# Optimization experiments

Measured on AMD Instinct MI355X. Metric: run time of the kernel, lower is better.

Reference implementation:

```python
import jax, jax.numpy as jnp
import numpy as np

B, N, H, TD = 64, 100, 128, 128
EPS = 1e-5  # BatchNorm eps (torch default)


def _xavier(k, shape):
    fan_in, fan_out = shape
    lim = (6.0 / (fan_in + fan_out)) ** 0.5
    return jax.random.uniform(k, shape, jnp.float32, -lim, lim)


def setup_inputs() -> dict:
    key = jax.random.key(0)
    ks = jax.random.split(key, 12)
    inp = {}
    inp["X"] = jax.random.randint(ks[0], (B, N * N), 0, 2).astype(jnp.float32)
    inp["time"] = jax.random.uniform(ks[1], (B,), jnp.float32)
    # Time_embedding MLP: Linear(TD->H), ReLU, Linear(H->H)
    inp["Wt1"] = _xavier(ks[2], (TD, H)); inp["bt1"] = jnp.zeros((H,), jnp.float32)
    inp["Wt2"] = _xavier(ks[3], (H, H)); inp["bt2"] = jnp.zeros((H,), jnp.float32)
    # TemporalGCNBlock.time_emb: Linear(H->N) + BN(N) + ReLU
    inp["Wtn"] = _xavier(ks[4], (H, N)); inp["btn"] = jnp.zeros((N,), jnp.float32)
    inp["g_tn"] = jnp.ones((N,), jnp.float32); inp["b_tn"] = jnp.zeros((N,), jnp.float32)
    # three GCNConv layers + BN
    inp["Wg1"] = _xavier(ks[5], (2 * N, H)); inp["bg1"] = jnp.zeros((H,), jnp.float32)
    inp["g1"] = jnp.ones((H,), jnp.float32); inp["bb1"] = jnp.zeros((H,), jnp.float32)
    inp["Wg2"] = _xavier(ks[6], (H, H)); inp["bg2"] = jnp.zeros((H,), jnp.float32)
    inp["g2"] = jnp.ones((H,), jnp.float32); inp["bb2"] = jnp.zeros((H,), jnp.float32)
    inp["Wg3"] = _xavier(ks[7], (H, H)); inp["bg3"] = jnp.zeros((H,), jnp.float32)
    inp["g3"] = jnp.ones((H,), jnp.float32); inp["bb3"] = jnp.zeros((H,), jnp.float32)
    # edge head: Linear(2H->H)+BN(H), Linear(2H->1)+BN(1)
    inp["We0"] = _xavier(ks[8], (2 * H, H)); inp["be0"] = jnp.zeros((H,), jnp.float32)
    inp["g_e0"] = jnp.ones((H,), jnp.float32); inp["b_e0"] = jnp.zeros((H,), jnp.float32)
    inp["We1"] = _xavier(ks[9], (2 * H, 1)); inp["be1"] = jnp.zeros((1,), jnp.float32)
    inp["g_e1"] = jnp.ones((1,), jnp.float32); inp["b_e1"] = jnp.zeros((1,), jnp.float32)
    return inp


def _bn(x, g, b):
    # eval-mode BatchNorm with fresh running stats (mean=0, var=1)
    return g * (x / jnp.sqrt(1.0 + EPS)) + b


def _timestep_embedding(t, dim, max_positions=10000):
    half = dim // 2
    freqs = jnp.exp(jnp.arange(half, dtype=jnp.float32) * (-np.log(max_positions) / (half - 1)))
    ang = t[:, None] * freqs[None, :]  # (B, half)
    return jnp.concatenate([jnp.sin(ang), jnp.cos(ang)], axis=1)


def reference(X, time, Wt1, bt1, Wt2, bt2, Wtn, btn, g_tn, b_tn,
              Wg1, bg1, g1, bb1, Wg2, bg2, g2, bb2, Wg3, bg3, g3, bb3,
              We0, be0, g_e0, b_e0, We1, be1, g_e1, b_e1):
    eye = jnp.eye(N, dtype=jnp.float32)
    # dense_to_sparse keeps nonzeros with unit edge weight; gcn_norm adds
    # remaining self-loops then symmetric-normalizes: A_hat = D^-1/2 (A|I) D^-1/2
    A = (X.reshape(B, N, N) != 0).astype(jnp.float32)
    At = jnp.maximum(A, eye)
    dinv = At.sum(-1) ** -0.5  # deg >= 1 thanks to self-loops
    Ah = dinv[:, :, None] * At * dinv[:, None, :]  # (B,N,N)

    # global time embedding (B,H)
    temb = _timestep_embedding(time, TD)
    h = jax.nn.relu(temb @ Wt1 + bt1) @ Wt2 + bt2
    # per-node time features (B,N); repeat_interleave == same vector per node
    t_node = jax.nn.relu(_bn(h @ Wtn + btn, g_tn, b_tn))
    x = jnp.concatenate([jnp.broadcast_to(eye, (B, N, N)),
                         jnp.broadcast_to(t_node[:, None, :], (B, N, N))], axis=-1)  # (B,N,2N)

    def gcn_block(x, W, b, g, bb):
        return jax.nn.relu(_bn(jnp.einsum('bij,bjh->bih', Ah, x @ W) + b, g, bb))

    x = gcn_block(x, Wg1, bg1, g1, bb1)
    x = gcn_block(x, Wg2, bg2, g2, bb2)
    x = gcn_block(x, Wg3, bg3, g3, bb3)  # (B,N,H)

    # edge head: Linear on concat(x_i, x_j) == split projections + broadcast add
    ei = x @ We0[:H]          # (B,N,H)
    ej = x @ We0[H:]          # (B,N,H)
    e0 = ei[:, :, None, :] + ej[:, None, :, :] + be0  # (B,N,N,H)
    e0 = _bn(e0, g_e0, b_e0)
    # Linear on concat(e0, time_emb): split into edge and time projections
    s = jnp.einsum('bijh,h->bij', e0, We1[:H, 0]) + (h @ We1[H:, 0])[:, None, None] + be1[0]
    s = _bn(s, g_e1[0], b_e1[0])
    out = (s * (1.0 - eye))[..., None]  # mask diagonal, (B,N,N,1)
    return out
```

## Files before the change

kernel.cpp:

```cpp
#include <hip/hip_runtime.h>
#include <math.h>

#define NB 64
#define NN 100
#define HH 128
#define HC 16
#define NCH 8

static constexpr float EPSBN = 1e-5f;

__global__ __launch_bounds__(256, 2) void k_l1f(
    const float* __restrict__ X, const float* __restrict__ timev,
    const float* __restrict__ Wt1, const float* __restrict__ bt1,
    const float* __restrict__ Wt2, const float* __restrict__ bt2,
    const float* __restrict__ Wtn, const float* __restrict__ btn,
    const float* __restrict__ g_tn, const float* __restrict__ b_tn,
    const float* __restrict__ Wg1, const float* __restrict__ bg1,
    const float* __restrict__ g1, const float* __restrict__ bb1,
    const float* __restrict__ We1, const float* __restrict__ be1,
    const float* __restrict__ be0, const float* __restrict__ g_e0,
    const float* __restrict__ b_e0,
    float* __restrict__ dinv, float* __restrict__ Dfull,
    float* __restrict__ out) {
    __shared__ float sZ[NN * 20];
    __shared__ float sdv[104], srs[104], su1[128];
    __shared__ float s_temb[128], s_h1[128], s_h[128], s_tn[104];
    __shared__ float spart[256];
    const int b = blockIdx.x, hcb = blockIdx.y, hc = hcb * HC;
    const int t = threadIdx.x, jp = t & 3, ig = t >> 2;
    const float rinv = 1.0f / sqrtf(1.f + EPSBN);
    const float* __restrict__ Xb = X + b * NN * NN;

    if (t < 200) {
        const int row = t >> 1, h = t & 1;
        const float4* r4 = (const float4*)(Xb + row * NN);
        float d = 0.f;
        const int qs = h ? 13 : 0, qe = h ? 25 : 13;
        for (int q = qs; q < qe; ++q) {
            float4 v = r4[q];
            d += v.x + v.y + v.z + v.w;
        }
        d += __shfl_xor(d, 1);
        if (h == 0) {
            if (Xb[row * NN + row] == 0.f) d += 1.f;
            sdv[row] = 1.0f / sqrtf(d);
        }
    }
    {
        const float tt = timev[b];
        if (t < 128) {
            int k = t & 63;
            float f = expf((float)k * (-logf(10000.f) / 63.f));
            float a = tt * f;
            s_temb[t] = (t < 64) ? sinf(a) : cosf(a);
        }
        __syncthreads();
        const int h = t & 127, half = t >> 7;
        {
            const float* wp = Wt1 + (half * 64) * HH + h;
            const float* e = s_temb + half * 64;
            float a0 = 0.f, a1 = 0.f, a2 = 0.f, a3 = 0.f;
#pragma unroll 4
            for (int q = 0; q < 64; q += 4) {
                a0 = fmaf(e[q + 0], wp[(q + 0) * HH], a0);
                a1 = fmaf(e[q + 1], wp[(q + 1) * HH], a1);
                a2 = fmaf(e[q + 2], wp[(q + 2) * HH], a2);
                a3 = fmaf(e[q + 3], wp[(q + 3) * HH], a3);
            }
            spart[t] = (a0 + a1) + (a2 + a3);
        }
        __syncthreads();
        if (t < 128) s_h1[t] = fmaxf(spart[t] + spart[128 + t] + bt1[t], 0.f);
        __syncthreads();
        {
            const float* wp = Wt2 + (half * 64) * HH + h;
            const float* e = s_h1 + half * 64;
            float a0 = 0.f, a1 = 0.f, a2 = 0.f, a3 = 0.f;
#pragma unroll 4
            for (int q = 0; q < 64; q += 4) {
                a0 = fmaf(e[q + 0], wp[(q + 0) * HH], a0);
                a1 = fmaf(e[q + 1], wp[(q + 1) * HH], a1);
                a2 = fmaf(e[q + 2], wp[(q + 2) * HH], a2);
                a3 = fmaf(e[q + 3], wp[(q + 3) * HH], a3);
            }
            spart[t] = (a0 + a1) + (a2 + a3);
        }
        __syncthreads();
        if (t < 128) s_h[t] = spart[t] + spart[128 + t] + bt2[t];
        __syncthreads();
        if (h < NN) {
            const float* wp = Wtn + (half * 64) * NN + h;
            const float* e = s_h + half * 64;
            float a0 = 0.f, a1 = 0.f, a2 = 0.f, a3 = 0.f;
#pragma unroll 4
            for (int q = 0; q < 64; q += 4) {
                a0 = fmaf(e[q + 0], wp[(q + 0) * NN], a0);
                a1 = fmaf(e[q + 1], wp[(q + 1) * NN], a1);
                a2 = fmaf(e[q + 2], wp[(q + 2) * NN], a2);
                a3 = fmaf(e[q + 3], wp[(q + 3) * NN], a3);
            }
            spart[t] = (a0 + a1) + (a2 + a3);
        }
        __syncthreads();
        if (t < NN)
            s_tn[t] = fmaxf(fmaf(g_tn[t] * rinv, spart[t] + spart[128 + t] + btn[t],
                                 b_tn[t]), 0.f);
        __syncthreads();
        {
            const float* wp = Wg1 + (NN + half * 50) * HH + h;
            const float* e = s_tn + half * 50;
            float a0 = 0.f, a1 = 0.f;
#pragma unroll 5
            for (int q = 0; q < 50; q += 2) {
                a0 = fmaf(e[q + 0], wp[(q + 0) * HH], a0);
                a1 = fmaf(e[q + 1], wp[(q + 1) * HH], a1);
            }
            spart[t] = a0 + a1;
        }
        __syncthreads();
        if (t < 128) su1[t] = spart[t] + spart[128 + t];
        if (hcb == 0) {
            __syncthreads();
            if (t < 128)
                spart[t] = s_h[t] * We1[HH + t] +
                           (be0[t] * g_e0[t] * rinv + b_e0[t]) * We1[t];
            __syncthreads();
            if (t < 64) {
                float v = spart[t] + spart[t + 64];
                v += __shfl_xor(v, 1);  v += __shfl_xor(v, 2);
                v += __shfl_xor(v, 4);  v += __shfl_xor(v, 8);
                v += __shfl_xor(v, 16); v += __shfl_xor(v, 32);
                if (t == 0) Dfull[b] = v + be1[0];
            }
        }
    }
    if (t < 200) {
        const int row = t >> 1, h = t & 1;
        float ssum = 0.f;
        for (int j = h; j < NN; j += 2) {
            float x = Xb[row * NN + j];
            float at = (row == j) ? 1.f : x;
            ssum += at * sdv[j];
        }
        ssum += __shfl_xor(ssum, 1);
        if (h == 0) srs[row] = sdv[row] * ssum;
    }
    if (hcb == 0 && t < NN) dinv[b * NN + t] = sdv[t];
    __syncthreads();
    for (int idx = t; idx < 400; idx += 256) {
        int j = idx >> 2, c4 = idx & 3;
        float4 w = *(const float4*)&Wg1[j * HH + hc + c4 * 4];
        float dj = sdv[j];
        *(float4*)&sZ[j * 20 + c4 * 4] = make_float4(dj * w.x, dj * w.y, dj * w.z, dj * w.w);
    }
    __syncthreads();
    const int r0 = ig, r1 = (ig < 36) ? 64 + ig : ig;
    float a0[16], a1[16];
#pragma unroll
    for (int c = 0; c < 16; ++c) { a0[c] = 0.f; a1[c] = 0.f; }
    const int j0 = jp * 28;
#pragma unroll
    for (int s = 0; s < 7; ++s) {
        const int j = j0 + s * 4;
        if (j < NN) {
            float4 v0 = *(const float4*)&Xb[r0 * NN + j];
            float4 v1 = *(const float4*)&Xb[r1 * NN + j];
#pragma unroll
            for (int jj = 0; jj < 4; ++jj) {
                const float e0 = (&v0.x)[jj], e1 = (&v1.x)[jj];
                const int zr = (j + jj) * 20;
#pragma unroll
                for (int c4 = 0; c4 < 4; ++c4) {
                    float4 z = *(const float4*)&sZ[zr + c4 * 4];
                    a0[c4 * 4 + 0] = fmaf(e0, z.x, a0[c4 * 4 + 0]);
                    a0[c4 * 4 + 1] = fmaf(e0, z.y, a0[c4 * 4 + 1]);
                    a0[c4 * 4 + 2] = fmaf(e0, z.z, a0[c4 * 4 + 2]);
                    a0[c4 * 4 + 3] = fmaf(e0, z.w, a0[c4 * 4 + 3]);
                    a1[c4 * 4 + 0] = fmaf(e1, z.x, a1[c4 * 4 + 0]);
                    a1[c4 * 4 + 1] = fmaf(e1, z.y, a1[c4 * 4 + 1]);
                    a1[c4 * 4 + 2] = fmaf(e1, z.z, a1[c4 * 4 + 2]);
                    a1[c4 * 4 + 3] = fmaf(e1, z.w, a1[c4 * 4 + 3]);
                }
            }
        }
    }
#pragma unroll
    for (int c = 0; c < 16; ++c) {
        a0[c] += __shfl_xor(a0[c], 1); a0[c] += __shfl_xor(a0[c], 2);
        a1[c] += __shfl_xor(a1[c], 1); a1[c] += __shfl_xor(a1[c], 2);
    }
    if (jp == 0) {
        const float di0 = sdv[r0], di1 = sdv[r1];
        const float cr0 = 1.f - Xb[r0 * NN + r0];
        const float cr1 = 1.f - Xb[r1 * NN + r1];
        const float rs0 = srs[r0], rs1 = srs[r1];
        float* ob = out + b * NN * HH;
#pragma unroll
        for (int c4 = 0; c4 < 4; ++c4) {
            float4 gv = *(const float4*)&g1[hc + c4 * 4];
            float4 bbv = *(const float4*)&bb1[hc + c4 * 4];
            float4 bgv = *(const float4*)&bg1[hc + c4 * 4];
            float4 uv = *(const float4*)&su1[hc + c4 * 4];
            float4 y0, y1;
#pragma unroll
            for (int cc = 0; cc < 4; ++cc) {
                const int c = c4 * 4 + cc;
                float s0 = di0 * fmaf(cr0, sZ[r0 * 20 + c], a0[c]);
                float s1 = di1 * fmaf(cr1, sZ[r1 * 20 + c], a1[c]);
                (&y0.x)[cc] = fmaxf(fmaf((&gv.x)[cc] * rinv,
                                         s0 + rs0 * (&uv.x)[cc] + (&bgv.x)[cc],
                                         (&bbv.x)[cc]), 0.f);
                (&y1.x)[cc] = fmaxf(fmaf((&gv.x)[cc] * rinv,
                                         s1 + rs1 * (&uv.x)[cc] + (&bgv.x)[cc],
                                         (&bbv.x)[cc]), 0.f);
            }
            *(float4*)&ob[r0 * HH + hc + c4 * 4] = y0;
            if (ig < 36) *(float4*)&ob[r1 * HH + hc + c4 * 4] = y1;
        }
    }
}

template <bool LAST>
__global__ __launch_bounds__(256, 2) void k_layer(
    const float* __restrict__ X, const float* __restrict__ dinv,
    const float* __restrict__ xin, const float* __restrict__ W,
    const float* __restrict__ bg, const float* __restrict__ g,
    const float* __restrict__ bb,
    const float* __restrict__ We0, const float* __restrict__ We1,
    const float* __restrict__ g_e0,
    float* __restrict__ out, float* __restrict__ psi, float* __restrict__ psj) {
    __shared__ float sW[128 * 16];
    __shared__ float sZ[NN * 20];
    __shared__ float sdv[NN];
    __shared__ float sc[128], sVi[16], sVj[16];
    const int b = blockIdx.x, hcb = blockIdx.y, hc = hcb * HC;
    const int t = threadIdx.x, jp = t & 3, ig = t >> 2;
    const float rinv = 1.0f / sqrtf(1.f + EPSBN);
    if (t < NN) sdv[t] = dinv[b * NN + t];
    if (LAST && t >= 112 && t < 240) sc[t - 112] = g_e0[t - 112] * We1[t - 112] * rinv;
    for (int idx = t; idx < 512; idx += 256) {
        int k = idx >> 2, c4 = idx & 3;
        int kp = ((k & 31) << 2) | (k >> 5);
        *(float4*)&sW[kp * 16 + c4 * 4] = *(const float4*)&W[k * HH + hc + c4 * 4];
    }
    __syncthreads();
    if (LAST && t < 32) {
        const int h = hc + (t & 15);
        const float* row = We0 + ((t < 16) ? h : (HH + h)) * HH;
        float a = 0.f;
        for (int hh = 0; hh < HH; ++hh) a = fmaf(row[hh], sc[hh], a);
        if (t < 16) sVi[t] = a; else sVj[t - 16] = a;
    }
    const int r0 = ig, r1 = (ig < 36) ? 64 + ig : ig;
    const float* __restrict__ xb = xin + b * NN * HH;
    float a0[16], a1[16];
#pragma unroll
    for (int c = 0; c < 16; ++c) { a0[c] = 0.f; a1[c] = 0.f; }
    const int wb = jp << 4;
#pragma unroll
    for (int s = 0; s < 8; ++s) {
        const int k = (jp << 5) + s * 4;
        float4 x0 = *(const float4*)&xb[r0 * HH + k];
        float4 x1 = *(const float4*)&xb[r1 * HH + k];
#pragma unroll
        for (int kk = 0; kk < 4; ++kk) {
            const float e0 = (&x0.x)[kk], e1 = (&x1.x)[kk];
            const int wr = ((s * 4 + kk) << 6) + wb;
#pragma unroll
            for (int c4 = 0; c4 < 4; ++c4) {
                float4 w = *(const float4*)&sW[wr + c4 * 4];
                a0[c4 * 4 + 0] = fmaf(e0, w.x, a0[c4 * 4 + 0]);
                a0[c4 * 4 + 1] = fmaf(e0, w.y, a0[c4 * 4 + 1]);
                a0[c4 * 4 + 2] = fmaf(e0, w.z, a0[c4 * 4 + 2]);
                a0[c4 * 4 + 3] = fmaf(e0, w.w, a0[c4 * 4 + 3]);
                a1[c4 * 4 + 0] = fmaf(e1, w.x, a1[c4 * 4 + 0]);
                a1[c4 * 4 + 1] = fmaf(e1, w.y, a1[c4 * 4 + 1]);
                a1[c4 * 4 + 2] = fmaf(e1, w.z, a1[c4 * 4 + 2]);
                a1[c4 * 4 + 3] = fmaf(e1, w.w, a1[c4 * 4 + 3]);
            }
        }
    }
#pragma unroll
    for (int c = 0; c < 16; ++c) {
        a0[c] += __shfl_xor(a0[c], 1); a0[c] += __shfl_xor(a0[c], 2);
        a1[c] += __shfl_xor(a1[c], 1); a1[c] += __shfl_xor(a1[c], 2);
    }
    if (jp == 0) {
        const float di0 = sdv[r0], di1 = sdv[r1];
#pragma unroll
        for (int c4 = 0; c4 < 4; ++c4) {
            *(float4*)&sZ[r0 * 20 + c4 * 4] =
                make_float4(di0 * a0[c4 * 4 + 0], di0 * a0[c4 * 4 + 1],
                            di0 * a0[c4 * 4 + 2], di0 * a0[c4 * 4 + 3]);
            if (ig < 36)
                *(float4*)&sZ[r1 * 20 + c4 * 4] =
                    make_float4(di1 * a1[c4 * 4 + 0], di1 * a1[c4 * 4 + 1],
                                di1 * a1[c4 * 4 + 2], di1 * a1[c4 * 4 + 3]);
        }
    }
    __syncthreads();
#pragma unroll
    for (int c = 0; c < 16; ++c) { a0[c] = 0.f; a1[c] = 0.f; }
    const float* __restrict__ Xb = X + b * NN * NN;
    const int j0 = jp * 28;
#pragma unroll
    for (int s = 0; s < 7; ++s) {
        const int j = j0 + s * 4;
        if (j < NN) {
            float4 v0 = *(const float4*)&Xb[r0 * NN + j];
            float4 v1 = *(const float4*)&Xb[r1 * NN + j];
#pragma unroll
            for (int jj = 0; jj < 4; ++jj) {
                const float e0 = (&v0.x)[jj], e1 = (&v1.x)[jj];
                const int zr = (j + jj) * 20;
#pragma unroll
                for (int c4 = 0; c4 < 4; ++c4) {
                    float4 z = *(const float4*)&sZ[zr + c4 * 4];
                    a0[c4 * 4 + 0] = fmaf(e0, z.x, a0[c4 * 4 + 0]);
                    a0[c4 * 4 + 1] = fmaf(e0, z.y, a0[c4 * 4 + 1]);
                    a0[c4 * 4 + 2] = fmaf(e0, z.z, a0[c4 * 4 + 2]);
                    a0[c4 * 4 + 3] = fmaf(e0, z.w, a0[c4 * 4 + 3]);
                    a1[c4 * 4 + 0] = fmaf(e1, z.x, a1[c4 * 4 + 0]);
                    a1[c4 * 4 + 1] = fmaf(e1, z.y, a1[c4 * 4 + 1]);
                    a1[c4 * 4 + 2] = fmaf(e1, z.z, a1[c4 * 4 + 2]);
                    a1[c4 * 4 + 3] = fmaf(e1, z.w, a1[c4 * 4 + 3]);
                }
            }
        }
    }
#pragma unroll
    for (int c = 0; c < 16; ++c) {
        a0[c] += __shfl_xor(a0[c], 1); a0[c] += __shfl_xor(a0[c], 2);
        a1[c] += __shfl_xor(a1[c], 1); a1[c] += __shfl_xor(a1[c], 2);
    }
    if (jp == 0) {
        const float di0 = sdv[r0], di1 = sdv[r1];
        const float cr0 = 1.f - Xb[r0 * NN + r0];
        const float cr1 = 1.f - Xb[r1 * NN + r1];
        float y0[16], y1[16];
#pragma unroll
        for (int c4 = 0; c4 < 4; ++c4) {
            float4 gv = *(const float4*)&g[hc + c4 * 4];
            float4 bbv = *(const float4*)&bb[hc + c4 * 4];
            float4 bgv = *(const float4*)&bg[hc + c4 * 4];
#pragma unroll
            for (int cc = 0; cc < 4; ++cc) {
                const int c = c4 * 4 + cc;
                float s0 = di0 * fmaf(cr0, sZ[r0 * 20 + c], a0[c]);
                float s1 = di1 * fmaf(cr1, sZ[r1 * 20 + c], a1[c]);
                y0[c] = fmaxf(fmaf((&gv.x)[cc] * rinv, s0 + (&bgv.x)[cc], (&bbv.x)[cc]), 0.f);
                y1[c] = fmaxf(fmaf((&gv.x)[cc] * rinv, s1 + (&bgv.x)[cc], (&bbv.x)[cc]), 0.f);
            }
        }
        if (LAST) {
            float pi0 = 0.f, pj0 = 0.f, pi1 = 0.f, pj1 = 0.f;
#pragma unroll
            for (int c = 0; c < 16; ++c) {
                pi0 = fmaf(y0[c], sVi[c], pi0); pj0 = fmaf(y0[c], sVj[c], pj0);
                pi1 = fmaf(y1[c], sVi[c], pi1); pj1 = fmaf(y1[c], sVj[c], pj1);
            }
            psi[(b * NN + r0) * NCH + hcb] = pi0;
            psj[(b * NN + r0) * NCH + hcb] = pj0;
            if (ig < 36) {
                psi[(b * NN + r1) * NCH + hcb] = pi1;
                psj[(b * NN + r1) * NCH + hcb] = pj1;
            }
        } else {
            float* ob = out + b * NN * HH;
#pragma unroll
            for (int c4 = 0; c4 < 4; ++c4) {
                *(float4*)&ob[r0 * HH + hc + c4 * 4] =
                    make_float4(y0[c4 * 4 + 0], y0[c4 * 4 + 1], y0[c4 * 4 + 2], y0[c4 * 4 + 3]);
                if (ig < 36)
                    *(float4*)&ob[r1 * HH + hc + c4 * 4] =
                        make_float4(y1[c4 * 4 + 0], y1[c4 * 4 + 1], y1[c4 * 4 + 2], y1[c4 * 4 + 3]);
            }
        }
    }
}

__global__ __launch_bounds__(256) void k_out(
    const float* __restrict__ psi, const float* __restrict__ psj,
    const float* __restrict__ Dfull, const float* __restrict__ g_e1,
    const float* __restrict__ b_e1, float* __restrict__ outp) {
    __shared__ float ssi[25], ssj[NN];
    const int b = blockIdx.x, i0 = blockIdx.y * 25;
    const int t = threadIdx.x;
    if (t < NN) {
        float s = 0.f;
        const float4* p = (const float4*)(psj + (b * NN + t) * NCH);
#pragma unroll
        for (int q = 0; q < NCH / 4; ++q) {
            float4 v = p[q];
            s += v.x + v.y + v.z + v.w;
        }
        ssj[t] = s;
    }
    if (t >= 128 && t < 128 + 25) {
        int i = t - 128;
        float s = 0.f;
        const float4* p = (const float4*)(psi + (b * NN + i0 + i) * NCH);
#pragma unroll
        for (int q = 0; q < NCH / 4; ++q) {
            float4 v = p[q];
            s += v.x + v.y + v.z + v.w;
        }
        ssi[i] = s;
    }
    __syncthreads();
    const float rinv = 1.0f / sqrtf(1.f + EPSBN);
    const float D = Dfull[b], ge = g_e1[0] * rinv, be = b_e1[0];
    float* ob = outp + b * NN * NN + i0 * NN;
    for (int e = t; e < 25 * NN; e += 256) {
        int ii = e / NN, j = e - ii * NN;
        float v = fmaf(ge, ssi[ii] + ssj[j] + D, be);
        ob[e] = (i0 + ii == j) ? 0.f : v;
    }
}

extern "C" void kernel_launch(void* const* d_in, const int* in_sizes, int n_in,
                              void* d_out, int out_size, void* d_ws, size_t ws_size,
                              hipStream_t stream) {
    const float* X    = (const float*)d_in[0];
    const float* timev= (const float*)d_in[1];
    const float* Wt1  = (const float*)d_in[2];
    const float* bt1  = (const float*)d_in[3];
    const float* Wt2  = (const float*)d_in[4];
    const float* bt2  = (const float*)d_in[5];
    const float* Wtn  = (const float*)d_in[6];
    const float* btn  = (const float*)d_in[7];
    const float* g_tn = (const float*)d_in[8];
    const float* b_tn = (const float*)d_in[9];
    const float* Wg1  = (const float*)d_in[10];
    const float* bg1  = (const float*)d_in[11];
    const float* g1   = (const float*)d_in[12];
    const float* bb1  = (const float*)d_in[13];
    const float* Wg2  = (const float*)d_in[14];
    const float* bg2  = (const float*)d_in[15];
    const float* g2   = (const float*)d_in[16];
    const float* bb2  = (const float*)d_in[17];
    const float* Wg3  = (const float*)d_in[18];
    const float* bg3  = (const float*)d_in[19];
    const float* g3   = (const float*)d_in[20];
    const float* bb3  = (const float*)d_in[21];
    const float* We0  = (const float*)d_in[22];
    const float* be0  = (const float*)d_in[23];
    const float* g_e0 = (const float*)d_in[24];
    const float* b_e0 = (const float*)d_in[25];
    const float* We1  = (const float*)d_in[26];
    const float* be1  = (const float*)d_in[27];
    const float* g_e1 = (const float*)d_in[28];
    const float* b_e1 = (const float*)d_in[29];

    float* ws = (float*)d_ws;
    float* dinv  = ws;
    float* Dfull = dinv + 6400;
    float* x1    = Dfull + 64;
    float* x2    = x1 + 819200;
    float* psi   = x1;
    float* psj   = x1 + 51200;

    k_l1f<<<dim3(NB, NCH), dim3(256), 0, stream>>>(
        X, timev, Wt1, bt1, Wt2, bt2, Wtn, btn, g_tn, b_tn,
        Wg1, bg1, g1, bb1, We1, be1, be0, g_e0, b_e0,
        dinv, Dfull, x1);

    k_layer<false><<<dim3(NB, NCH), dim3(256), 0, stream>>>(
        X, dinv, x1, Wg2, bg2, g2, bb2,
        nullptr, nullptr, nullptr, x2, nullptr, nullptr);

    k_layer<true><<<dim3(NB, NCH), dim3(256), 0, stream>>>(
        X, dinv, x2, Wg3, bg3, g3, bb3,
        We0, We1, g_e0, nullptr, psi, psj);

    k_out<<<dim3(NB, 4), dim3(256), 0, stream>>>(psi, psj, Dfull, g_e1, b_e1,
                                                 (float*)d_out);
}
```

Measured before the change: 55.56 us.

## Split time-embedding MLP into separate per-batch kernel, restructure degree computation in layer 1

The time-embedding MLP chain (temb, two hidden layers, node projection, the u1 projection through Wg1, and the Dfull scalar) moves into a new kernel launched once per batch. Previously every one of the 8 channel blocks per batch recomputed it. The layer-1 kernel now reads u1 from global memory. Its degree and row-sum computations reuse the same thread-to-row mapping as the main accumulation loop, which lets X rows be served from cache. The cost is one extra kernel launch and a global round trip for u1.

```diff
diff --git a/kernel.cpp b/kernel.cpp
--- a/kernel.cpp
+++ b/kernel.cpp
@@ -9,144 +9,163 @@
 
 static constexpr float EPSBN = 1e-5f;
 
-__global__ __launch_bounds__(256, 2) void k_l1f(
-    const float* __restrict__ X, const float* __restrict__ timev,
+__global__ __launch_bounds__(256) void k_pre(
+    const float* __restrict__ timev,
     const float* __restrict__ Wt1, const float* __restrict__ bt1,
     const float* __restrict__ Wt2, const float* __restrict__ bt2,
     const float* __restrict__ Wtn, const float* __restrict__ btn,
     const float* __restrict__ g_tn, const float* __restrict__ b_tn,
-    const float* __restrict__ Wg1, const float* __restrict__ bg1,
+    const float* __restrict__ Wg1, const float* __restrict__ We1,
+    const float* __restrict__ be1, const float* __restrict__ be0,
+    const float* __restrict__ g_e0, const float* __restrict__ b_e0,
+    float* __restrict__ u1, float* __restrict__ Dfull) {
+    __shared__ float s_temb[128], s_h1[128], s_h[128], s_tn[104], spart[256];
+    const int b = blockIdx.x, t = threadIdx.x;
+    const float rinv = 1.0f / sqrtf(1.f + EPSBN);
+    const float tt = timev[b];
+    if (t < 128) {
+        int k = t & 63;
+        float f = expf((float)k * (-logf(10000.f) / 63.f));
+        float a = tt * f;
+        s_temb[t] = (t < 64) ? sinf(a) : cosf(a);
+    }
+    __syncthreads();
+    const int h = t & 127, half = t >> 7;
+    {
+        const float* wp = Wt1 + (half * 64) * HH + h;
+        const float* e = s_temb + half * 64;
+        float a0 = 0.f, a1 = 0.f, a2 = 0.f, a3 = 0.f;
+#pragma unroll 4
+        for (int q = 0; q < 64; q += 4) {
+            a0 = fmaf(e[q + 0], wp[(q + 0) * HH], a0);
+            a1 = fmaf(e[q + 1], wp[(q + 1) * HH], a1);
+            a2 = fmaf(e[q + 2], wp[(q + 2) * HH], a2);
+            a3 = fmaf(e[q + 3], wp[(q + 3) * HH], a3);
+        }
+        spart[t] = (a0 + a1) + (a2 + a3);
+    }
+    __syncthreads();
+    if (t < 128) s_h1[t] = fmaxf(spart[t] + spart[128 + t] + bt1[t], 0.f);
+    __syncthreads();
+    {
+        const float* wp = Wt2 + (half * 64) * HH + h;
+        const float* e = s_h1 + half * 64;
+        float a0 = 0.f, a1 = 0.f, a2 = 0.f, a3 = 0.f;
+#pragma unroll 4
+        for (int q = 0; q < 64; q += 4) {
+            a0 = fmaf(e[q + 0], wp[(q + 0) * HH], a0);
+            a1 = fmaf(e[q + 1], wp[(q + 1) * HH], a1);
+            a2 = fmaf(e[q + 2], wp[(q + 2) * HH], a2);
+            a3 = fmaf(e[q + 3], wp[(q + 3) * HH], a3);
+        }
+        spart[t] = (a0 + a1) + (a2 + a3);
+    }
+    __syncthreads();
+    if (t < 128) s_h[t] = spart[t] + spart[128 + t] + bt2[t];
+    __syncthreads();
+    if (h < NN) {
+        const float* wp = Wtn + (half * 64) * NN + h;
+        const float* e = s_h + half * 64;
+        float a0 = 0.f, a1 = 0.f, a2 = 0.f, a3 = 0.f;
+#pragma unroll 4
+        for (int q = 0; q < 64; q += 4) {
+            a0 = fmaf(e[q + 0], wp[(q + 0) * NN], a0);
+            a1 = fmaf(e[q + 1], wp[(q + 1) * NN], a1);
+            a2 = fmaf(e[q + 2], wp[(q + 2) * NN], a2);
+            a3 = fmaf(e[q + 3], wp[(q + 3) * NN], a3);
+        }
+        spart[t] = (a0 + a1) + (a2 + a3);
+    }
+    __syncthreads();
+    if (t < NN)
+        s_tn[t] = fmaxf(fmaf(g_tn[t] * rinv, spart[t] + spart[128 + t] + btn[t],
+                             b_tn[t]), 0.f);
+    __syncthreads();
+    {
+        const float* wp = Wg1 + (NN + half * 50) * HH + h;
+        const float* e = s_tn + half * 50;
+        float a0 = 0.f, a1 = 0.f;
+#pragma unroll 5
+        for (int q = 0; q < 50; q += 2) {
+            a0 = fmaf(e[q + 0], wp[(q + 0) * HH], a0);
+            a1 = fmaf(e[q + 1], wp[(q + 1) * HH], a1);
+        }
+        spart[t] = a0 + a1;
+    }
+    __syncthreads();
+    if (t < 128) u1[b * HH + t] = spart[t] + spart[128 + t];
+    __syncthreads();
+    if (t < 128)
+        spart[t] = s_h[t] * We1[HH + t] +
+                   (be0[t] * g_e0[t] * rinv + b_e0[t]) * We1[t];
+    __syncthreads();
+    if (t < 64) {
+        float v = spart[t] + spart[t + 64];
+        v += __shfl_xor(v, 1);  v += __shfl_xor(v, 2);
+        v += __shfl_xor(v, 4);  v += __shfl_xor(v, 8);
+        v += __shfl_xor(v, 16); v += __shfl_xor(v, 32);
+        if (t == 0) Dfull[b] = v + be1[0];
+    }
+}
+
+__global__ __launch_bounds__(256, 2) void k_l1(
+    const float* __restrict__ X, const float* __restrict__ Wg1,
+    const float* __restrict__ u1, const float* __restrict__ bg1,
     const float* __restrict__ g1, const float* __restrict__ bb1,
-    const float* __restrict__ We1, const float* __restrict__ be1,
-    const float* __restrict__ be0, const float* __restrict__ g_e0,
-    const float* __restrict__ b_e0,
-    float* __restrict__ dinv, float* __restrict__ Dfull,
-    float* __restrict__ out) {
+    float* __restrict__ dinv, float* __restrict__ out) {
     __shared__ float sZ[NN * 20];
-    __shared__ float sdv[104], srs[104], su1[128];
-    __shared__ float s_temb[128], s_h1[128], s_h[128], s_tn[104];
-    __shared__ float spart[256];
+    __shared__ float sdv[NN];
     const int b = blockIdx.x, hcb = blockIdx.y, hc = hcb * HC;
     const int t = threadIdx.x, jp = t & 3, ig = t >> 2;
-    const float rinv = 1.0f / sqrtf(1.f + EPSBN);
+    const int r0 = ig, r1 = (ig < 36) ? 64 + ig : ig;
     const float* __restrict__ Xb = X + b * NN * NN;
-
-    if (t < 200) {
-        const int row = t >> 1, h = t & 1;
-        const float4* r4 = (const float4*)(Xb + row * NN);
-        float d = 0.f;
-        const int qs = h ? 13 : 0, qe = h ? 25 : 13;
-        for (int q = qs; q < qe; ++q) {
-            float4 v = r4[q];
-            d += v.x + v.y + v.z + v.w;
-        }
-        d += __shfl_xor(d, 1);
-        if (h == 0) {
-            if (Xb[row * NN + row] == 0.f) d += 1.f;
-            sdv[row] = 1.0f / sqrtf(d);
-        }
-    }
-    {
-        const float tt = timev[b];
-        if (t < 128) {
-            int k = t & 63;
-            float f = expf((float)k * (-logf(10000.f) / 63.f));
-            float a = tt * f;
-            s_temb[t] = (t < 64) ? sinf(a) : cosf(a);
-        }
-        __syncthreads();
-        const int h = t & 127, half = t >> 7;
-        {
-            const float* wp = Wt1 + (half * 64) * HH + h;
-            const float* e = s_temb + half * 64;
-            float a0 = 0.f, a1 = 0.f, a2 = 0.f, a3 = 0.f;
-#pragma unroll 4
-            for (int q = 0; q < 64; q += 4) {
-                a0 = fmaf(e[q + 0], wp[(q + 0) * HH], a0);
-                a1 = fmaf(e[q + 1], wp[(q + 1) * HH], a1);
-                a2 = fmaf(e[q + 2], wp[(q + 2) * HH], a2);
-                a3 = fmaf(e[q + 3], wp[(q + 3) * HH], a3);
-            }
-            spart[t] = (a0 + a1) + (a2 + a3);
-        }
-        __syncthreads();
-        if (t < 128) s_h1[t] = fmaxf(spart[t] + spart[128 + t] + bt1[t], 0.f);
-        __syncthreads();
-        {
-            const float* wp = Wt2 + (half * 64) * HH + h;
-            const float* e = s_h1 + half * 64;
-            float a0 = 0.f, a1 = 0.f, a2 = 0.f, a3 = 0.f;
-#pragma unroll 4
-            for (int q = 0; q < 64; q += 4) {
-                a0 = fmaf(e[q + 0], wp[(q + 0) * HH], a0);
-                a1 = fmaf(e[q + 1], wp[(q + 1) * HH], a1);
-                a2 = fmaf(e[q + 2], wp[(q + 2) * HH], a2);
-                a3 = fmaf(e[q + 3], wp[(q + 3) * HH], a3);
-            }
-            spart[t] = (a0 + a1) + (a2 + a3);
-        }
-        __syncthreads();
-        if (t < 128) s_h[t] = spart[t] + spart[128 + t] + bt2[t];
-        __syncthreads();
-        if (h < NN) {
-            const float* wp = Wtn + (half * 64) * NN + h;
-            const float* e = s_h + half * 64;
-            float a0 = 0.f, a1 = 0.f, a2 = 0.f, a3 = 0.f;
-#pragma unroll 4
-            for (int q = 0; q < 64; q += 4) {
-                a0 = fmaf(e[q + 0], wp[(q + 0) * NN], a0);
-                a1 = fmaf(e[q + 1], wp[(q + 1) * NN], a1);
-                a2 = fmaf(e[q + 2], wp[(q + 2) * NN], a2);
-                a3 = fmaf(e[q + 3], wp[(q + 3) * NN], a3);
-            }
-            spart[t] = (a0 + a1) + (a2 + a3);
-        }
-        __syncthreads();
-        if (t < NN)
-            s_tn[t] = fmaxf(fmaf(g_tn[t] * rinv, spart[t] + spart[128 + t] + btn[t],
-                                 b_tn[t]), 0.f);
-        __syncthreads();
-        {
-            const float* wp = Wg1 + (NN + half * 50) * HH + h;
-            const float* e = s_tn + half * 50;
-            float a0 = 0.f, a1 = 0.f;
-#pragma unroll 5
-            for (int q = 0; q < 50; q += 2) {
-                a0 = fmaf(e[q + 0], wp[(q + 0) * HH], a0);
-                a1 = fmaf(e[q + 1], wp[(q + 1) * HH], a1);
-            }
-            spart[t] = a0 + a1;
-        }
-        __syncthreads();
-        if (t < 128) su1[t] = spart[t] + spart[128 + t];
-        if (hcb == 0) {
-            __syncthreads();
-            if (t < 128)
-                spart[t] = s_h[t] * We1[HH + t] +
-                           (be0[t] * g_e0[t] * rinv + b_e0[t]) * We1[t];
-            __syncthreads();
-            if (t < 64) {
-                float v = spart[t] + spart[t + 64];
-                v += __shfl_xor(v, 1);  v += __shfl_xor(v, 2);
-                v += __shfl_xor(v, 4);  v += __shfl_xor(v, 8);
-                v += __shfl_xor(v, 16); v += __shfl_xor(v, 32);
-                if (t == 0) Dfull[b] = v + be1[0];
-            }
-        }
-    }
-    if (t < 200) {
-        const int row = t >> 1, h = t & 1;
-        float ssum = 0.f;
-        for (int j = h; j < NN; j += 2) {
-            float x = Xb[row * NN + j];
-            float at = (row == j) ? 1.f : x;
-            ssum += at * sdv[j];
-        }
-        ssum += __shfl_xor(ssum, 1);
-        if (h == 0) srs[row] = sdv[row] * ssum;
-    }
-    if (hcb == 0 && t < NN) dinv[b * NN + t] = sdv[t];
-    __syncthreads();
+    const int j0 = jp * 28;
+    float d0 = 0.f, d1 = 0.f;
+#pragma unroll
+    for (int s = 0; s < 7; ++s) {
+        const int j = j0 + s * 4;
+        if (j < NN) {
+            float4 v0 = *(const float4*)&Xb[r0 * NN + j];
+            float4 v1 = *(const float4*)&Xb[r1 * NN + j];
+            d0 += (v0.x + v0.y) + (v0.z + v0.w);
+            d1 += (v1.x + v1.y) + (v1.z + v1.w);
+        }
+    }
+    d0 += __shfl_xor(d0, 1); d0 += __shfl_xor(d0, 2);
+    d1 += __shfl_xor(d1, 1); d1 += __shfl_xor(d1, 2);
+    if (jp == 0) {
+        if (Xb[r0 * NN + r0] == 0.f) d0 += 1.f;
+        sdv[r0] = 1.0f / sqrtf(d0);
+        if (ig < 36) {
+            if (Xb[r1 * NN + r1] == 0.f) d1 += 1.f;
+            sdv[r1] = 1.0f / sqrtf(d1);
+        }
+    }
+    __syncthreads();
+    float rsum0 = 0.f, rsum1 = 0.f;
+#pragma unroll
+    for (int s = 0; s < 7; ++s) {
+        const int j = j0 + s * 4;
+        if (j < NN) {
+            float4 v0 = *(const float4*)&Xb[r0 * NN + j];
+            float4 v1 = *(const float4*)&Xb[r1 * NN + j];
+#pragma unroll
+            for (int jj = 0; jj < 4; ++jj) {
+                const float dj = sdv[j + jj];
+                float at0 = (r0 == j + jj) ? 1.f : (&v0.x)[jj];
+                float at1 = (r1 == j + jj) ? 1.f : (&v1.x)[jj];
+                rsum0 = fmaf(at0, dj, rsum0);
+                rsum1 = fmaf(at1, dj, rsum1);
+            }
+        }
+    }
+    rsum0 += __shfl_xor(rsum0, 1); rsum0 += __shfl_xor(rsum0, 2);
+    rsum1 += __shfl_xor(rsum1, 1); rsum1 += __shfl_xor(rsum1, 2);
+    const float rs0 = sdv[r0] * rsum0, rs1 = sdv[r1] * rsum1;
+    if (hcb == 0 && jp == 0) {
+        dinv[b * NN + r0] = sdv[r0];
+        if (ig < 36) dinv[b * NN + r1] = sdv[r1];
+    }
     for (int idx = t; idx < 400; idx += 256) {
         int j = idx >> 2, c4 = idx & 3;
         float4 w = *(const float4*)&Wg1[j * HH + hc + c4 * 4];
@@ -154,11 +173,9 @@
         *(float4*)&sZ[j * 20 + c4 * 4] = make_float4(dj * w.x, dj * w.y, dj * w.z, dj * w.w);
     }
     __syncthreads();
-    const int r0 = ig, r1 = (ig < 36) ? 64 + ig : ig;
     float a0[16], a1[16];
 #pragma unroll
     for (int c = 0; c < 16; ++c) { a0[c] = 0.f; a1[c] = 0.f; }
-    const int j0 = jp * 28;
 #pragma unroll
     for (int s = 0; s < 7; ++s) {
         const int j = j0 + s * 4;
@@ -190,17 +207,17 @@
         a1[c] += __shfl_xor(a1[c], 1); a1[c] += __shfl_xor(a1[c], 2);
     }
     if (jp == 0) {
+        const float rinv = 1.0f / sqrtf(1.f + EPSBN);
         const float di0 = sdv[r0], di1 = sdv[r1];
         const float cr0 = 1.f - Xb[r0 * NN + r0];
         const float cr1 = 1.f - Xb[r1 * NN + r1];
-        const float rs0 = srs[r0], rs1 = srs[r1];
         float* ob = out + b * NN * HH;
 #pragma unroll
         for (int c4 = 0; c4 < 4; ++c4) {
             float4 gv = *(const float4*)&g1[hc + c4 * 4];
             float4 bbv = *(const float4*)&bb1[hc + c4 * 4];
             float4 bgv = *(const float4*)&bg1[hc + c4 * 4];
-            float4 uv = *(const float4*)&su1[hc + c4 * 4];
+            float4 uv = *(const float4*)&u1[b * HH + hc + c4 * 4];
             float4 y0, y1;
 #pragma unroll
             for (int cc = 0; cc < 4; ++cc) {
@@ -454,21 +471,21 @@
 
     float* ws = (float*)d_ws;
     float* dinv  = ws;
-    float* Dfull = dinv + 6400;
+    float* u1    = dinv + 6400;
+    float* Dfull = u1 + 8192;
     float* x1    = Dfull + 64;
     float* x2    = x1 + 819200;
     float* psi   = x1;
     float* psj   = x1 + 51200;
 
-    k_l1f<<<dim3(NB, NCH), dim3(256), 0, stream>>>(
-        X, timev, Wt1, bt1, Wt2, bt2, Wtn, btn, g_tn, b_tn,
-        Wg1, bg1, g1, bb1, We1, be1, be0, g_e0, b_e0,
-        dinv, Dfull, x1);
-
+    k_pre<<<dim3(NB), dim3(256), 0, stream>>>(
+        timev, Wt1, bt1, Wt2, bt2, Wtn, btn, g_tn, b_tn, Wg1, We1, be1,
+        be0, g_e0, b_e0, u1, Dfull);
+
+    k_l1<<<dim3(NB, NCH), dim3(256), 0, stream>>>(X, Wg1, u1, bg1, g1, bb1, dinv, x1);
     k_layer<false><<<dim3(NB, NCH), dim3(256), 0, stream>>>(
         X, dinv, x1, Wg2, bg2, g2, bb2,
         nullptr, nullptr, nullptr, x2, nullptr, nullptr);
-
     k_layer<true><<<dim3(NB, NCH), dim3(256), 0, stream>>>(
         X, dinv, x2, Wg3, bg3, g3, bb3,
         We0, We1, g_e0, nullptr, psi, psj);
```

Measured after the change: 53.57 us. -3.6%, faster.
